# Kernel tuning notes

Measured on AMD Instinct MI355X. Metric: run time of the kernel, lower is better.

Reference implementation:

```python
import jax, jax.numpy as jnp
import numpy as np

TEMP = 0.05


def _l2norm(x, axis=-1, eps=1e-12):
    n = jnp.sqrt(jnp.sum(x * x, axis=axis, keepdims=True))
    return x / jnp.maximum(n, eps)


def setup_inputs() -> dict:
    key = jax.random.key(0)
    k1, k2, k3 = jax.random.split(key, 3)
    B, D, N = 1024, 2048, 16384
    inputs = jax.random.normal(k1, (B, D), dtype=jnp.float32)
    targets = jax.random.randint(k2, (B,), 0, N, dtype=jnp.int32).astype(jnp.int64)
    # cluster memory bank: initialized to unit-norm centroids (buffer is zeros in
    # torch but is always filled with normalized centroids before use)
    features = _l2norm(jax.random.normal(k3, (N, D), dtype=jnp.float32))
    return {"inputs": inputs, "targets": targets, "features": features}


def reference(inputs, targets, features):
    # ClusterMemory.forward: normalize -> cosine sim vs bank -> / temp
    xn = _l2norm(inputs, axis=1)            # [B, D]
    out = (xn @ features.T) / TEMP          # [B, N]
    return out
```

## Files before the change

### kernel.cpp

```cpp
#include <hip/hip_runtime.h>
#include <hip/hip_bf16.h>


typedef short bf16x8 __attribute__((ext_vector_type(8)));
typedef float f32x4  __attribute__((ext_vector_type(4)));

#define D_K   2048
#define N_N   16384
#define M_M   1024
#define TEMP_INV 20.0f

__device__ __forceinline__ unsigned short f2bf(float f) {
    unsigned u = __builtin_bit_cast(unsigned, f);
    u += 0x7FFFu + ((u >> 16) & 1u);
    return (unsigned short)(u >> 16);
}

#define GLOAD16(g, l) __builtin_amdgcn_global_load_lds(                        \
    (const __attribute__((address_space(1))) unsigned int*)(g),                \
    (__attribute__((address_space(3))) unsigned int*)(l), 16, 0, 0)

__global__ __launch_bounds__(256) void prep_kernel(const float* __restrict__ x,
                                                   const float* __restrict__ B,
                                                   unsigned short* __restrict__ abf,
                                                   unsigned short* __restrict__ bbf) {
    int t = threadIdx.x;
    if (blockIdx.x < M_M) {
        int row = blockIdx.x;
        const float4* xr = reinterpret_cast<const float4*>(x + (size_t)row * D_K);
        float4 a = xr[t * 2];
        float4 b = xr[t * 2 + 1];
        float s = a.x*a.x + a.y*a.y + a.z*a.z + a.w*a.w
                + b.x*b.x + b.y*b.y + b.z*b.z + b.w*b.w;
        #pragma unroll
        for (int off = 32; off > 0; off >>= 1) s += __shfl_down(s, off);
        __shared__ float ps[4];
        __shared__ float sbc;
        if ((t & 63) == 0) ps[t >> 6] = s;
        __syncthreads();
        if (t == 0) {
            float tot = ps[0] + ps[1] + ps[2] + ps[3];
            sbc = 1.0f / fmaxf(sqrtf(tot), 1e-12f);
        }
        __syncthreads();
        float rs = sbc;
        bf16x8 v;
        v[0] = (short)f2bf(a.x * rs); v[1] = (short)f2bf(a.y * rs);
        v[2] = (short)f2bf(a.z * rs); v[3] = (short)f2bf(a.w * rs);
        v[4] = (short)f2bf(b.x * rs); v[5] = (short)f2bf(b.y * rs);
        v[6] = (short)f2bf(b.z * rs); v[7] = (short)f2bf(b.w * rs);
        *reinterpret_cast<bf16x8*>(abf + (size_t)row * D_K + t * 8) = v;
    } else {
        const size_t nv = (size_t)N_N * D_K / 8;
        size_t stride = (size_t)(gridDim.x - M_M) * blockDim.x;
        for (size_t v = (size_t)(blockIdx.x - M_M) * blockDim.x + t; v < nv; v += stride) {
            const float4* p = reinterpret_cast<const float4*>(B) + v * 2;
            float4 a = p[0], b = p[1];
            bf16x8 o;
            o[0] = (short)f2bf(a.x); o[1] = (short)f2bf(a.y);
            o[2] = (short)f2bf(a.z); o[3] = (short)f2bf(a.w);
            o[4] = (short)f2bf(b.x); o[5] = (short)f2bf(b.y);
            o[6] = (short)f2bf(b.z); o[7] = (short)f2bf(b.w);
            reinterpret_cast<bf16x8*>(bbf)[v] = o;
        }
    }
}

__global__ __launch_bounds__(512, 2) void gemm8_kernel(const unsigned short* __restrict__ Abf,
                                                       const unsigned short* __restrict__ Bbf,
                                                       float* __restrict__ C) {
    __shared__ __align__(16) unsigned short lds[65536];

    int bid = blockIdx.x;
    int wg  = (bid & 7) * 32 + (bid >> 3);
    int tm  = wg & 3, tn = wg >> 2;
    int m_blk = tm * 256, n_blk = tn * 256;

    int t = threadIdx.x, lane = t & 63, w = t >> 6;
    int wm = w >> 2, wn = w & 3;

    int l15  = lane & 15;
    int slot = ((lane >> 4) ^ ((l15 >> 1) & 3)) * 16;
    int aoff = (wm * 128 + l15) * 64 + slot;
    int boff = (wn * 64  + l15) * 64 + slot;

    const unsigned short* gA[2];
    const unsigned short* gB[2];
    int sdst[2];
    #pragma unroll
    for (int pass = 0; pass < 2; ++pass) {
        int r = pass * 128 + (t >> 2);
        int csrc = (t & 3) ^ ((r >> 1) & 3);
        gA[pass] = Abf + (size_t)(m_blk + r) * D_K + csrc * 8;
        gB[pass] = Bbf + (size_t)(n_blk + r) * D_K + csrc * 8;
        sdst[pass] = pass * 8192 + w * 1024;
    }

    auto stage = [&](int mat, int s, int b, int ktile) {
        int kt = ktile < 32 ? ktile : 31;
        int koff = kt * 64 + s * 32;
        int ldsb = b * 65536 + mat * 32768 + s * 16384;
        GLOAD16((mat ? gB[0] : gA[0]) + koff, (char*)lds + ldsb + sdst[0]);
        GLOAD16((mat ? gB[1] : gA[1]) + koff, (char*)lds + ldsb + sdst[1]);
    };

    f32x4 acc[8][4] = {};
    bf16x8 bfr[4];

#define PHASE(b, mh, s, LOADB, stMat, stS, stB, stKt, VM)                      \
    {                                                                          \
        bf16x8 af[4];                                                          \
        _Pragma("unroll")                                                      \
        for (int f = 0; f < 4; ++f)                                            \
            af[f] = *reinterpret_cast<const bf16x8*>(                          \
                (char*)lds + (b) * 65536 + (s) * 16384 + aoff +                \
                ((mh) * 64 + f * 16) * 64);                                    \
        if (LOADB) {                                                           \
            _Pragma("unroll")                                                  \
            for (int n = 0; n < 4; ++n)                                        \
                bfr[n] = *reinterpret_cast<const bf16x8*>(                     \
                    (char*)lds + (b) * 65536 + 32768 + (s) * 16384 + boff +    \
                    n * 1024);                                                 \
        }                                                                      \
        stage(stMat, stS, stB, stKt);                                          \
        asm volatile("s_barrier" ::: "memory");                                \
        asm volatile("s_waitcnt lgkmcnt(0)" ::: "memory");                     \
        __builtin_amdgcn_sched_barrier(0);                                     \
        __builtin_amdgcn_s_setprio(1);                                         \
        _Pragma("unroll")                                                      \
        for (int f = 0; f < 4; ++f) {                                          \
            _Pragma("unroll")                                                  \
            for (int n = 0; n < 4; ++n)                                        \
                acc[(mh) * 4 + f][n] = __builtin_amdgcn_mfma_f32_16x16x32_bf16(\
                    af[f], bfr[n], acc[(mh) * 4 + f][n], 0, 0, 0);             \
        }                                                                      \
        __builtin_amdgcn_s_setprio(0);                                         \
        if (VM) asm volatile("s_waitcnt vmcnt(8)" ::: "memory");               \
        asm volatile("s_barrier" ::: "memory");                                \
    }

    stage(0, 0, 0, 0);
    stage(1, 0, 0, 0);
    stage(0, 1, 0, 0);
    stage(1, 1, 0, 0);
    stage(0, 0, 1, 1);
    stage(1, 0, 1, 1);
    asm volatile("s_waitcnt vmcnt(8)" ::: "memory");
    asm volatile("s_barrier" ::: "memory");

    for (int u = 0; u < 16; ++u) {
        int t1 = 2 * u + 1;
        PHASE(0, 0, 0, true,  0, 1, 1, t1,     false)
        PHASE(0, 1, 0, false, 1, 1, 1, t1,     true )
        PHASE(0, 0, 1, true,  0, 0, 0, t1 + 1, false)
        PHASE(0, 1, 1, false, 1, 0, 0, t1 + 1, true )
        PHASE(1, 0, 0, true,  0, 1, 0, t1 + 1, false)
        PHASE(1, 1, 0, false, 1, 1, 0, t1 + 1, true )
        PHASE(1, 0, 1, true,  0, 0, 1, t1 + 2, false)
        PHASE(1, 1, 1, false, 1, 0, 1, t1 + 2, true )
    }
#undef PHASE

    #pragma unroll
    for (int f = 0; f < 8; ++f) {
        int r = m_blk + wm * 128 + (f >> 2) * 64 + (f & 3) * 16 + (lane >> 4) * 4;
        #pragma unroll
        for (int j = 0; j < 4; ++j) {
            float* cp = C + (size_t)(r + j) * N_N + n_blk + wn * 64 + (lane & 15);
            #pragma unroll
            for (int n = 0; n < 4; ++n)
                cp[n * 16] = acc[f][n][j] * TEMP_INV;
        }
    }
}

__global__ __launch_bounds__(256) void rnorm_kernel(const float* __restrict__ x,
                                                    float* __restrict__ rn) {
    int row = blockIdx.x;
    const float4* xr = reinterpret_cast<const float4*>(x + (size_t)row * D_K);
    int t = threadIdx.x;
    float4 a = xr[t];
    float4 b = xr[t + 256];
    float s = a.x*a.x + a.y*a.y + a.z*a.z + a.w*a.w
            + b.x*b.x + b.y*b.y + b.z*b.z + b.w*b.w;
    #pragma unroll
    for (int off = 32; off > 0; off >>= 1) s += __shfl_down(s, off);
    __shared__ float ps[4];
    int wave = t >> 6, lane = t & 63;
    if (lane == 0) ps[wave] = s;
    __syncthreads();
    if (t == 0) {
        float tot = ps[0] + ps[1] + ps[2] + ps[3];
        rn[row] = 1.0f / fmaxf(sqrtf(tot), 1e-12f);
    }
}

__global__ __launch_bounds__(256, 2) void gemm_kernel(const float* __restrict__ A,
                                                      const float* __restrict__ Bm,
                                                      const float* __restrict__ rn,
                                                      float* __restrict__ C) {
    constexpr int BK = 64;
    __shared__ __align__(16) short lAs[128 * BK];
    __shared__ __align__(16) short lBs[128 * BK];
    int bid = blockIdx.x;
    int nb  = (bid & 7) * 128 + (bid >> 3);
    int tm  = nb & 7;
    int tn  = nb >> 3;
    int m0 = tm * 128, n0 = tn * 128;
    int t = threadIdx.x;
    int lane = t & 63, w = t >> 6;
    int wr = (w >> 1) * 64, wc = (w & 1) * 64;
    f32x4 acc[4][4] = {};
    float4 ra[4][2], rb[4][2];
    float  sc[4];
    int    srow[4], sgrp[4];
    #pragma unroll
    for (int i = 0; i < 4; ++i) {
        int li = t + i * 256;
        srow[i] = li >> 3;
        sgrp[i] = li & 7;
        sc[i]   = rn[m0 + srow[i]];
    }
    auto load_tiles = [&](int kt) {
        int k0 = kt * BK;
        #pragma unroll
        for (int i = 0; i < 4; ++i) {
            const float4* pa = reinterpret_cast<const float4*>(
                A + (size_t)(m0 + srow[i]) * D_K + k0 + sgrp[i] * 8);
            ra[i][0] = pa[0]; ra[i][1] = pa[1];
            const float4* pb = reinterpret_cast<const float4*>(
                Bm + (size_t)(n0 + srow[i]) * D_K + k0 + sgrp[i] * 8);
            rb[i][0] = pb[0]; rb[i][1] = pb[1];
        }
    };
    auto write_tiles = [&]() {
        #pragma unroll
        for (int i = 0; i < 4; ++i) {
            int row = srow[i];
            int slotw = sgrp[i] ^ (row & 7);
            float s = sc[i];
            bf16x8 va, vb;
            va[0] = (short)f2bf(ra[i][0].x * s); va[1] = (short)f2bf(ra[i][0].y * s);
            va[2] = (short)f2bf(ra[i][0].z * s); va[3] = (short)f2bf(ra[i][0].w * s);
            va[4] = (short)f2bf(ra[i][1].x * s); va[5] = (short)f2bf(ra[i][1].y * s);
            va[6] = (short)f2bf(ra[i][1].z * s); va[7] = (short)f2bf(ra[i][1].w * s);
        vb[0] = (short)f2bf(rb[i][0].x); vb[1] = (short)f2bf(rb[i][0].y);
        vb[2] = (short)f2bf(rb[i][0].z); vb[3] = (short)f2bf(rb[i][0].w);
        vb[4] = (short)f2bf(rb[i][1].x); vb[5] = (short)f2bf(rb[i][1].y);
        vb[6] = (short)f2bf(rb[i][1].z); vb[7] = (short)f2bf(rb[i][1].w);
            *reinterpret_cast<bf16x8*>(&lAs[row * BK + slotw * 8]) = va;
            *reinterpret_cast<bf16x8*>(&lBs[row * BK + slotw * 8]) = vb;
        }
    };
    auto compute = [&]() {
        #pragma unroll
        for (int ks = 0; ks < 2; ++ks) {
            bf16x8 af[4], bfr[4];
            #pragma unroll
            for (int f = 0; f < 4; ++f) {
                int arow = wr + f * 16 + (lane & 15);
                int aslot = (ks * 4 + (lane >> 4)) ^ (arow & 7);
                af[f] = *reinterpret_cast<const bf16x8*>(&lAs[arow * BK + aslot * 8]);
                int brow = wc + f * 16 + (lane & 15);
                int bslot = (ks * 4 + (lane >> 4)) ^ (brow & 7);
                bfr[f] = *reinterpret_cast<const bf16x8*>(&lBs[brow * BK + bslot * 8]);
            }
            #pragma unroll
            for (int m = 0; m < 4; ++m)
                #pragma unroll
                for (int n = 0; n < 4; ++n)
                    acc[m][n] = __builtin_amdgcn_mfma_f32_16x16x32_bf16(
                        af[m], bfr[n], acc[m][n], 0, 0, 0);
        }
    };
    load_tiles(0);
    write_tiles();
    for (int kt = 1; kt < D_K / BK; ++kt) {
        __syncthreads();
        load_tiles(kt);
        compute();
        __syncthreads();
        write_tiles();
    }
    __syncthreads();
    compute();
    #pragma unroll
    for (int m = 0; m < 4; ++m) {
        int r = m0 + wr + m * 16 + (lane >> 4) * 4;
        #pragma unroll
        for (int j = 0; j < 4; ++j) {
            float* cp = C + (size_t)(r + j) * N_N + n0 + wc + (lane & 15);
            #pragma unroll
            for (int n = 0; n < 4; ++n)
                cp[n * 16] = acc[m][n][j] * TEMP_INV;
        }
    }
}

extern "C" void kernel_launch(void* const* d_in, const int* in_sizes, int n_in,
                              void* d_out, int out_size, void* d_ws, size_t ws_size,
                              hipStream_t stream) {
    const float* inputs   = (const float*)d_in[0];
    const float* features = (const float*)d_in[2];
    float* out = (float*)d_out;

    const size_t needA = (size_t)M_M * D_K * 2;
    const size_t needB = (size_t)N_N * D_K * 2;
    if (ws_size >= needA + needB) {
        unsigned short* Abf = (unsigned short*)d_ws;
        unsigned short* Bbf = Abf + (size_t)M_M * D_K;
        prep_kernel<<<M_M + 2048, 256, 0, stream>>>(inputs, features, Abf, Bbf);
        gemm8_kernel<<<(M_M / 256) * (N_N / 256), 512, 0, stream>>>(Abf, Bbf, out);
    } else {
        float* rn = (float*)d_ws;
        rnorm_kernel<<<M_M, 256, 0, stream>>>(inputs, rn);
        gemm_kernel<<<(M_M / 128) * (N_N / 128), 256, 0, stream>>>(inputs, features, rn, out);
    }
}
```

Before: 103.8 us.

## Replace eight-phase interleaved GEMM pipeline with simple per-tile double-buffered loop

Replaces the fine-grained eight-phase schedule, which interleaved half-tile global-to-LDS loads with MFMA batches under setprio, with a simpler loop. Each iteration loads the full k-tile fragments from LDS, runs all 64 MFMAs, and then stages the next tile into the same buffer after a barrier. This cuts the barrier count and simplifies the schedule. In exchange it needs more registers for fragments and overlaps global loads with compute less finely, since loads are issued only after compute on that buffer finishes.

```diff
diff --git a/kernel.cpp b/kernel.cpp
--- a/kernel.cpp
+++ b/kernel.cpp
@@ -96,70 +96,67 @@
         sdst[pass] = pass * 8192 + w * 1024;
     }
 
-    auto stage = [&](int mat, int s, int b, int ktile) {
+    auto stageTile = [&](int b, int ktile) {
         int kt = ktile < 32 ? ktile : 31;
-        int koff = kt * 64 + s * 32;
-        int ldsb = b * 65536 + mat * 32768 + s * 16384;
-        GLOAD16((mat ? gB[0] : gA[0]) + koff, (char*)lds + ldsb + sdst[0]);
-        GLOAD16((mat ? gB[1] : gA[1]) + koff, (char*)lds + ldsb + sdst[1]);
+        #pragma unroll
+        for (int s = 0; s < 2; ++s) {
+            int koff = kt * 64 + s * 32;
+            GLOAD16(gA[0] + koff, (char*)lds + b * 65536 + s * 16384 + sdst[0]);
+            GLOAD16(gA[1] + koff, (char*)lds + b * 65536 + s * 16384 + sdst[1]);
+            GLOAD16(gB[0] + koff, (char*)lds + b * 65536 + 32768 + s * 16384 + sdst[0]);
+            GLOAD16(gB[1] + koff, (char*)lds + b * 65536 + 32768 + s * 16384 + sdst[1]);
+        }
     };
 
     f32x4 acc[8][4] = {};
-    bf16x8 bfr[4];
-
-#define PHASE(b, mh, s, LOADB, stMat, stS, stB, stKt, VM)                      \
-    {                                                                          \
-        bf16x8 af[4];                                                          \
-        _Pragma("unroll")                                                      \
-        for (int f = 0; f < 4; ++f)                                            \
-            af[f] = *reinterpret_cast<const bf16x8*>(                          \
-                (char*)lds + (b) * 65536 + (s) * 16384 + aoff +                \
-                ((mh) * 64 + f * 16) * 64);                                    \
-        if (LOADB) {                                                           \
-            _Pragma("unroll")                                                  \
-            for (int n = 0; n < 4; ++n)                                        \
-                bfr[n] = *reinterpret_cast<const bf16x8*>(                     \
-                    (char*)lds + (b) * 65536 + 32768 + (s) * 16384 + boff +    \
-                    n * 1024);                                                 \
-        }                                                                      \
-        stage(stMat, stS, stB, stKt);                                          \
-        asm volatile("s_barrier" ::: "memory");                                \
-        asm volatile("s_waitcnt lgkmcnt(0)" ::: "memory");                     \
-        __builtin_amdgcn_sched_barrier(0);                                     \
-        __builtin_amdgcn_s_setprio(1);                                         \
-        _Pragma("unroll")                                                      \
-        for (int f = 0; f < 4; ++f) {                                          \
-            _Pragma("unroll")                                                  \
-            for (int n = 0; n < 4; ++n)                                        \
-                acc[(mh) * 4 + f][n] = __builtin_amdgcn_mfma_f32_16x16x32_bf16(\
-                    af[f], bfr[n], acc[(mh) * 4 + f][n], 0, 0, 0);             \
-        }                                                                      \
-        __builtin_amdgcn_s_setprio(0);                                         \
-        if (VM) asm volatile("s_waitcnt vmcnt(8)" ::: "memory");               \
-        asm volatile("s_barrier" ::: "memory");                                \
-    }
-
-    stage(0, 0, 0, 0);
-    stage(1, 0, 0, 0);
-    stage(0, 1, 0, 0);
-    stage(1, 1, 0, 0);
-    stage(0, 0, 1, 1);
-    stage(1, 0, 1, 1);
+
+    stageTile(0, 0);
+    stageTile(1, 1);
     asm volatile("s_waitcnt vmcnt(8)" ::: "memory");
     asm volatile("s_barrier" ::: "memory");
 
-    for (int u = 0; u < 16; ++u) {
-        int t1 = 2 * u + 1;
-        PHASE(0, 0, 0, true,  0, 1, 1, t1,     false)
-        PHASE(0, 1, 0, false, 1, 1, 1, t1,     true )
-        PHASE(0, 0, 1, true,  0, 0, 0, t1 + 1, false)
-        PHASE(0, 1, 1, false, 1, 0, 0, t1 + 1, true )
-        PHASE(1, 0, 0, true,  0, 1, 0, t1 + 1, false)
-        PHASE(1, 1, 0, false, 1, 1, 0, t1 + 1, true )
-        PHASE(1, 0, 1, true,  0, 0, 1, t1 + 2, false)
-        PHASE(1, 1, 1, false, 1, 0, 1, t1 + 2, true )
-    }
-#undef PHASE
+    for (int T = 0; T < 32; ++T) {
+        int b = T & 1;
+        char* base = (char*)lds + b * 65536;
+
+        bf16x8 a0[8], b0[4], a1[8], b1[4];
+        #pragma unroll
+        for (int ff = 0; ff < 8; ++ff)
+            a0[ff] = *reinterpret_cast<const bf16x8*>(
+                base + aoff + (((ff >> 2) * 64 + (ff & 3) * 16) * 64));
+        #pragma unroll
+        for (int n = 0; n < 4; ++n)
+            b0[n] = *reinterpret_cast<const bf16x8*>(
+                base + 32768 + boff + n * 1024);
+        #pragma unroll
+        for (int ff = 0; ff < 8; ++ff)
+            a1[ff] = *reinterpret_cast<const bf16x8*>(
+                base + 16384 + aoff + (((ff >> 2) * 64 + (ff & 3) * 16) * 64));
+        #pragma unroll
+        for (int n = 0; n < 4; ++n)
+            b1[n] = *reinterpret_cast<const bf16x8*>(
+                base + 32768 + 16384 + boff + n * 1024);
+
+        #pragma unroll
+        for (int ff = 0; ff < 8; ++ff)
+            #pragma unroll
+            for (int n = 0; n < 4; ++n)
+                acc[ff][n] = __builtin_amdgcn_mfma_f32_16x16x32_bf16(
+                    a0[ff], b0[n], acc[ff][n], 0, 0, 0);
+        #pragma unroll
+        for (int ff = 0; ff < 8; ++ff)
+            #pragma unroll
+            for (int n = 0; n < 4; ++n)
+                acc[ff][n] = __builtin_amdgcn_mfma_f32_16x16x32_bf16(
+                    a1[ff], b1[n], acc[ff][n], 0, 0, 0);
+
+        asm volatile("s_waitcnt lgkmcnt(0)" ::: "memory");
+        __builtin_amdgcn_sched_barrier(0);
+        asm volatile("s_barrier" ::: "memory");
+        stageTile(b, T + 2);
+        asm volatile("s_waitcnt vmcnt(8)" ::: "memory");
+        asm volatile("s_barrier" ::: "memory");
+    }
 
     #pragma unroll
     for (int f = 0; f < 8; ++f) {
@@ -244,10 +241,10 @@
             va[2] = (short)f2bf(ra[i][0].z * s); va[3] = (short)f2bf(ra[i][0].w * s);
             va[4] = (short)f2bf(ra[i][1].x * s); va[5] = (short)f2bf(ra[i][1].y * s);
             va[6] = (short)f2bf(ra[i][1].z * s); va[7] = (short)f2bf(ra[i][1].w * s);
-        vb[0] = (short)f2bf(rb[i][0].x); vb[1] = (short)f2bf(rb[i][0].y);
-        vb[2] = (short)f2bf(rb[i][0].z); vb[3] = (short)f2bf(rb[i][0].w);
-        vb[4] = (short)f2bf(rb[i][1].x); vb[5] = (short)f2bf(rb[i][1].y);
-        vb[6] = (short)f2bf(rb[i][1].z); vb[7] = (short)f2bf(rb[i][1].w);
+            vb[0] = (short)f2bf(rb[i][0].x); vb[1] = (short)f2bf(rb[i][0].y);
+            vb[2] = (short)f2bf(rb[i][0].z); vb[3] = (short)f2bf(rb[i][0].w);
+            vb[4] = (short)f2bf(rb[i][1].x); vb[5] = (short)f2bf(rb[i][1].y);
+            vb[6] = (short)f2bf(rb[i][1].z); vb[7] = (short)f2bf(rb[i][1].w);
             *reinterpret_cast<bf16x8*>(&lAs[row * BK + slotw * 8]) = va;
             *reinterpret_cast<bf16x8*>(&lBs[row * BK + slotw * 8]) = vb;
         }
```

Result: slower. 116.4 us (+12.1%).

## Switch GEMM to 32x32x16 bf16 MFMA with fewer, coarser pipeline phases

Applied to the files above, without the earlier changes.

The main GEMM kernel now uses 32x32x16 bf16 MFMA instructions with 16-float accumulators in place of 16x16x32. Each wave covers its 128x64 tile with 4x2 blocks and reads operands for both k-halves per phase. The pipeline drops from eight phases per two k-tiles to two phases per k-tile, each issuing two stage loads and one barrier pair. This cuts LDS reads per MFMA and barrier count, at the cost of larger operand register use per phase and a less coalesced column-strided epilogue.

```diff
diff --git a/kernel.cpp b/kernel.cpp
--- a/kernel.cpp
+++ b/kernel.cpp
@@ -2,8 +2,9 @@
 #include <hip/hip_bf16.h>
 
 
-typedef short bf16x8 __attribute__((ext_vector_type(8)));
-typedef float f32x4  __attribute__((ext_vector_type(4)));
+typedef short  bf16x8 __attribute__((ext_vector_type(8)));
+typedef float  f32x4  __attribute__((ext_vector_type(4)));
+typedef float  f32x16 __attribute__((ext_vector_type(16)));
 
 #define D_K   2048
 #define N_N   16384
@@ -66,9 +67,9 @@
     }
 }
 
-__global__ __launch_bounds__(512, 2) void gemm8_kernel(const unsigned short* __restrict__ Abf,
-                                                       const unsigned short* __restrict__ Bbf,
-                                                       float* __restrict__ C) {
+__global__ __launch_bounds__(512, 2) void gemm32_kernel(const unsigned short* __restrict__ Abf,
+                                                        const unsigned short* __restrict__ Bbf,
+                                                        float* __restrict__ C) {
     __shared__ __align__(16) unsigned short lds[65536];
 
     int bid = blockIdx.x;
@@ -79,10 +80,15 @@
     int t = threadIdx.x, lane = t & 63, w = t >> 6;
     int wm = w >> 2, wn = w & 3;
 
-    int l15  = lane & 15;
-    int slot = ((lane >> 4) ^ ((l15 >> 1) & 3)) * 16;
-    int aoff = (wm * 128 + l15) * 64 + slot;
-    int boff = (wn * 64  + l15) * 64 + slot;
+    int row31 = lane & 31, khalf = lane >> 5;
+    int xorm  = (row31 >> 1) & 3;
+    int slotk[2], aao[4], bbo[2];
+    #pragma unroll
+    for (int kk = 0; kk < 2; ++kk) slotk[kk] = ((kk * 2 + khalf) ^ xorm) * 16;
+    #pragma unroll
+    for (int rb = 0; rb < 4; ++rb) aao[rb] = (wm * 128 + rb * 32 + row31) * 64;
+    #pragma unroll
+    for (int cb = 0; cb < 2; ++cb) bbo[cb] = (wn * 64 + cb * 32 + row31) * 64;
 
     const unsigned short* gA[2];
     const unsigned short* gB[2];
@@ -104,38 +110,41 @@
         GLOAD16((mat ? gB[1] : gA[1]) + koff, (char*)lds + ldsb + sdst[1]);
     };
 
-    f32x4 acc[8][4] = {};
-    bf16x8 bfr[4];
-
-#define PHASE(b, mh, s, LOADB, stMat, stS, stB, stKt, VM)                      \
+    f32x16 acc[4][2] = {};
+
+#define PHASE32(bb, ss, ST1, ST2)                                              \
     {                                                                          \
-        bf16x8 af[4];                                                          \
+        char* abase = (char*)lds + (bb) * 65536 + (ss) * 16384;                \
+        char* bbase = abase + 32768;                                           \
+        bf16x8 af[4][2], bv[2][2];                                             \
         _Pragma("unroll")                                                      \
-        for (int f = 0; f < 4; ++f)                                            \
-            af[f] = *reinterpret_cast<const bf16x8*>(                          \
-                (char*)lds + (b) * 65536 + (s) * 16384 + aoff +                \
-                ((mh) * 64 + f * 16) * 64);                                    \
-        if (LOADB) {                                                           \
+        for (int rb = 0; rb < 4; ++rb)                                         \
             _Pragma("unroll")                                                  \
-            for (int n = 0; n < 4; ++n)                                        \
-                bfr[n] = *reinterpret_cast<const bf16x8*>(                     \
-                    (char*)lds + (b) * 65536 + 32768 + (s) * 16384 + boff +    \
-                    n * 1024);                                                 \
-        }                                                                      \
-        stage(stMat, stS, stB, stKt);                                          \
+            for (int kk = 0; kk < 2; ++kk)                                     \
+                af[rb][kk] = *reinterpret_cast<const bf16x8*>(                 \
+                    abase + aao[rb] + slotk[kk]);                              \
+        _Pragma("unroll")                                                      \
+        for (int cb = 0; cb < 2; ++cb)                                         \
+            _Pragma("unroll")                                                  \
+            for (int kk = 0; kk < 2; ++kk)                                     \
+                bv[cb][kk] = *reinterpret_cast<const bf16x8*>(                 \
+                    bbase + bbo[cb] + slotk[kk]);                              \
+        ST1;                                                                   \
+        ST2;                                                                   \
         asm volatile("s_barrier" ::: "memory");                                \
         asm volatile("s_waitcnt lgkmcnt(0)" ::: "memory");                     \
         __builtin_amdgcn_sched_barrier(0);                                     \
         __builtin_amdgcn_s_setprio(1);                                         \
         _Pragma("unroll")                                                      \
-        for (int f = 0; f < 4; ++f) {                                          \
+        for (int kk = 0; kk < 2; ++kk)                                         \
             _Pragma("unroll")                                                  \
-            for (int n = 0; n < 4; ++n)                                        \
-                acc[(mh) * 4 + f][n] = __builtin_amdgcn_mfma_f32_16x16x32_bf16(\
-                    af[f], bfr[n], acc[(mh) * 4 + f][n], 0, 0, 0);             \
-        }                                                                      \
+            for (int rb = 0; rb < 4; ++rb)                                     \
+                _Pragma("unroll")                                              \
+                for (int cb = 0; cb < 2; ++cb)                                 \
+                    acc[rb][cb] = __builtin_amdgcn_mfma_f32_32x32x16_bf16(     \
+                        af[rb][kk], bv[cb][kk], acc[rb][cb], 0, 0, 0);         \
         __builtin_amdgcn_s_setprio(0);                                         \
-        if (VM) asm volatile("s_waitcnt vmcnt(8)" ::: "memory");               \
+        asm volatile("s_waitcnt vmcnt(8)" ::: "memory");                       \
         asm volatile("s_barrier" ::: "memory");                                \
     }
 
@@ -148,30 +157,25 @@
     asm volatile("s_waitcnt vmcnt(8)" ::: "memory");
     asm volatile("s_barrier" ::: "memory");
 
-    for (int u = 0; u < 16; ++u) {
-        int t1 = 2 * u + 1;
-        PHASE(0, 0, 0, true,  0, 1, 1, t1,     false)
-        PHASE(0, 1, 0, false, 1, 1, 1, t1,     true )
-        PHASE(0, 0, 1, true,  0, 0, 0, t1 + 1, false)
-        PHASE(0, 1, 1, false, 1, 0, 0, t1 + 1, true )
-        PHASE(1, 0, 0, true,  0, 1, 0, t1 + 1, false)
-        PHASE(1, 1, 0, false, 1, 1, 0, t1 + 1, true )
-        PHASE(1, 0, 1, true,  0, 0, 1, t1 + 2, false)
-        PHASE(1, 1, 1, false, 1, 0, 1, t1 + 2, true )
-    }
-#undef PHASE
-
-    #pragma unroll
-    for (int f = 0; f < 8; ++f) {
-        int r = m_blk + wm * 128 + (f >> 2) * 64 + (f & 3) * 16 + (lane >> 4) * 4;
-        #pragma unroll
-        for (int j = 0; j < 4; ++j) {
-            float* cp = C + (size_t)(r + j) * N_N + n_blk + wn * 64 + (lane & 15);
+    for (int T = 0; T < 32; ++T) {
+        int b = T & 1;
+        PHASE32(b, 0, stage(0, 1, b ^ 1, T + 1), stage(1, 1, b ^ 1, T + 1))
+        PHASE32(b, 1, stage(0, 0, b,     T + 2), stage(1, 0, b,     T + 2))
+    }
+#undef PHASE32
+
+    #pragma unroll
+    for (int rb = 0; rb < 4; ++rb)
+        #pragma unroll
+        for (int cb = 0; cb < 2; ++cb) {
+            int colg = n_blk + wn * 64 + cb * 32 + row31;
             #pragma unroll
-            for (int n = 0; n < 4; ++n)
-                cp[n * 16] = acc[f][n][j] * TEMP_INV;
-        }
-    }
+            for (int r = 0; r < 16; ++r) {
+                int rowg = m_blk + wm * 128 + rb * 32 +
+                           (r & 3) + 8 * (r >> 2) + 4 * khalf;
+                C[(size_t)rowg * N_N + colg] = acc[rb][cb][r] * TEMP_INV;
+            }
+        }
 }
 
 __global__ __launch_bounds__(256) void rnorm_kernel(const float* __restrict__ x,
@@ -244,10 +248,10 @@
             va[2] = (short)f2bf(ra[i][0].z * s); va[3] = (short)f2bf(ra[i][0].w * s);
             va[4] = (short)f2bf(ra[i][1].x * s); va[5] = (short)f2bf(ra[i][1].y * s);
             va[6] = (short)f2bf(ra[i][1].z * s); va[7] = (short)f2bf(ra[i][1].w * s);
-        vb[0] = (short)f2bf(rb[i][0].x); vb[1] = (short)f2bf(rb[i][0].y);
-        vb[2] = (short)f2bf(rb[i][0].z); vb[3] = (short)f2bf(rb[i][0].w);
-        vb[4] = (short)f2bf(rb[i][1].x); vb[5] = (short)f2bf(rb[i][1].y);
-        vb[6] = (short)f2bf(rb[i][1].z); vb[7] = (short)f2bf(rb[i][1].w);
+            vb[0] = (short)f2bf(rb[i][0].x); vb[1] = (short)f2bf(rb[i][0].y);
+            vb[2] = (short)f2bf(rb[i][0].z); vb[3] = (short)f2bf(rb[i][0].w);
+            vb[4] = (short)f2bf(rb[i][1].x); vb[5] = (short)f2bf(rb[i][1].y);
+            vb[6] = (short)f2bf(rb[i][1].z); vb[7] = (short)f2bf(rb[i][1].w);
             *reinterpret_cast<bf16x8*>(&lAs[row * BK + slotw * 8]) = va;
             *reinterpret_cast<bf16x8*>(&lBs[row * BK + slotw * 8]) = vb;
         }
@@ -310,7 +314,7 @@
         unsigned short* Abf = (unsigned short*)d_ws;
         unsigned short* Bbf = Abf + (size_t)M_M * D_K;
         prep_kernel<<<M_M + 2048, 256, 0, stream>>>(inputs, features, Abf, Bbf);
-        gemm8_kernel<<<(M_M / 256) * (N_N / 256), 512, 0, stream>>>(Abf, Bbf, out);
+        gemm32_kernel<<<(M_M / 256) * (N_N / 256), 512, 0, stream>>>(Abf, Bbf, out);
     } else {
         float* rn = (float*)d_ws;
         rnorm_kernel<<<M_M, 256, 0, stream>>>(inputs, rn);
```

Result: slower. 113.2 us (+9.0%).

## Restructure GEMM main loop into four coarser phases per K-tile pair

Applied to the files above, without the earlier changes.

Replaces the eight-phase ping-pong schedule, which split each k-substep into two M halves, with four phases. Each phase loads all eight A fragments and four B fragments, issues both A and B stage loads, and runs 32 MFMAs. This halves the number of barriers and waitcnt points per K tile, reducing sync overhead. In exchange it holds more fragment registers live, which may pressure occupancy at 2 waves/SIMD, and gives coarser overlap between loads and MFMAs.

```diff
diff --git a/kernel.cpp b/kernel.cpp
--- a/kernel.cpp
+++ b/kernel.cpp
@@ -66,7 +66,7 @@
     }
 }
 
-__global__ __launch_bounds__(512, 2) void gemm8_kernel(const unsigned short* __restrict__ Abf,
+__global__ __launch_bounds__(512, 2) void gemm4_kernel(const unsigned short* __restrict__ Abf,
                                                        const unsigned short* __restrict__ Bbf,
                                                        float* __restrict__ C) {
     __shared__ __align__(16) unsigned short lds[65536];
@@ -81,8 +81,11 @@
 
     int l15  = lane & 15;
     int slot = ((lane >> 4) ^ ((l15 >> 1) & 3)) * 16;
-    int aoff = (wm * 128 + l15) * 64 + slot;
-    int boff = (wn * 64  + l15) * 64 + slot;
+    int aoff[8], boff;
+    #pragma unroll
+    for (int f = 0; f < 8; ++f)
+        aoff[f] = (wm * 128 + f * 16 + l15) * 64 + slot;
+    boff = (wn * 64 + l15) * 64 + slot;
 
     const unsigned short* gA[2];
     const unsigned short* gB[2];
@@ -105,37 +108,34 @@
     };
 
     f32x4 acc[8][4] = {};
-    bf16x8 bfr[4];
-
-#define PHASE(b, mh, s, LOADB, stMat, stS, stB, stKt, VM)                      \
+
+#define PHASE4(b, s, stS, stB, stKt)                                           \
     {                                                                          \
-        bf16x8 af[4];                                                          \
+        bf16x8 af[8], bfr[4];                                                  \
         _Pragma("unroll")                                                      \
-        for (int f = 0; f < 4; ++f)                                            \
+        for (int f = 0; f < 8; ++f)                                            \
             af[f] = *reinterpret_cast<const bf16x8*>(                          \
-                (char*)lds + (b) * 65536 + (s) * 16384 + aoff +                \
-                ((mh) * 64 + f * 16) * 64);                                    \
-        if (LOADB) {                                                           \
-            _Pragma("unroll")                                                  \
-            for (int n = 0; n < 4; ++n)                                        \
-                bfr[n] = *reinterpret_cast<const bf16x8*>(                     \
-                    (char*)lds + (b) * 65536 + 32768 + (s) * 16384 + boff +    \
-                    n * 1024);                                                 \
-        }                                                                      \
-        stage(stMat, stS, stB, stKt);                                          \
+                (char*)lds + (b) * 65536 + (s) * 16384 + aoff[f]);             \
+        _Pragma("unroll")                                                      \
+        for (int n = 0; n < 4; ++n)                                            \
+            bfr[n] = *reinterpret_cast<const bf16x8*>(                         \
+                (char*)lds + (b) * 65536 + 32768 + (s) * 16384 + boff +        \
+                n * 1024);                                                     \
+        stage(0, stS, stB, stKt);                                              \
+        stage(1, stS, stB, stKt);                                              \
         asm volatile("s_barrier" ::: "memory");                                \
         asm volatile("s_waitcnt lgkmcnt(0)" ::: "memory");                     \
         __builtin_amdgcn_sched_barrier(0);                                     \
         __builtin_amdgcn_s_setprio(1);                                         \
         _Pragma("unroll")                                                      \
-        for (int f = 0; f < 4; ++f) {                                          \
+        for (int f = 0; f < 8; ++f) {                                          \
             _Pragma("unroll")                                                  \
             for (int n = 0; n < 4; ++n)                                        \
-                acc[(mh) * 4 + f][n] = __builtin_amdgcn_mfma_f32_16x16x32_bf16(\
-                    af[f], bfr[n], acc[(mh) * 4 + f][n], 0, 0, 0);             \
+                acc[f][n] = __builtin_amdgcn_mfma_f32_16x16x32_bf16(           \
+                    af[f], bfr[n], acc[f][n], 0, 0, 0);                        \
         }                                                                      \
         __builtin_amdgcn_s_setprio(0);                                         \
-        if (VM) asm volatile("s_waitcnt vmcnt(8)" ::: "memory");               \
+        asm volatile("s_waitcnt vmcnt(8)" ::: "memory");                       \
         asm volatile("s_barrier" ::: "memory");                                \
     }
 
@@ -148,25 +148,19 @@
     asm volatile("s_waitcnt vmcnt(8)" ::: "memory");
     asm volatile("s_barrier" ::: "memory");
 
-    for (int u = 0; u < 16; ++u) {
-        int t1 = 2 * u + 1;
-        PHASE(0, 0, 0, true,  0, 1, 1, t1,     false)
-        PHASE(0, 1, 0, false, 1, 1, 1, t1,     true )
-        PHASE(0, 0, 1, true,  0, 0, 0, t1 + 1, false)
-        PHASE(0, 1, 1, false, 1, 0, 0, t1 + 1, true )
-        PHASE(1, 0, 0, true,  0, 1, 0, t1 + 1, false)
-        PHASE(1, 1, 0, false, 1, 1, 0, t1 + 1, true )
-        PHASE(1, 0, 1, true,  0, 0, 1, t1 + 2, false)
-        PHASE(1, 1, 1, false, 1, 0, 1, t1 + 2, true )
-    }
-#undef PHASE
+    for (int T = 0; T < 32; ++T) {
+        int b = T & 1;
+        PHASE4(b, 0, 1, b ^ 1, T + 1)
+        PHASE4(b, 1, 0, b,     T + 2)
+    }
+#undef PHASE4
 
     #pragma unroll
     for (int f = 0; f < 8; ++f) {
-        int r = m_blk + wm * 128 + (f >> 2) * 64 + (f & 3) * 16 + (lane >> 4) * 4;
+        int r = m_blk + wm * 128 + f * 16 + (lane >> 4) * 4;
         #pragma unroll
         for (int j = 0; j < 4; ++j) {
-            float* cp = C + (size_t)(r + j) * N_N + n_blk + wn * 64 + (lane & 15);
+            float* cp = C + (size_t)(r + j) * N_N + n_blk + wn * 64 + l15;
             #pragma unroll
             for (int n = 0; n < 4; ++n)
                 cp[n * 16] = acc[f][n][j] * TEMP_INV;
@@ -244,10 +238,10 @@
             va[2] = (short)f2bf(ra[i][0].z * s); va[3] = (short)f2bf(ra[i][0].w * s);
             va[4] = (short)f2bf(ra[i][1].x * s); va[5] = (short)f2bf(ra[i][1].y * s);
             va[6] = (short)f2bf(ra[i][1].z * s); va[7] = (short)f2bf(ra[i][1].w * s);
-        vb[0] = (short)f2bf(rb[i][0].x); vb[1] = (short)f2bf(rb[i][0].y);
-        vb[2] = (short)f2bf(rb[i][0].z); vb[3] = (short)f2bf(rb[i][0].w);
-        vb[4] = (short)f2bf(rb[i][1].x); vb[5] = (short)f2bf(rb[i][1].y);
-        vb[6] = (short)f2bf(rb[i][1].z); vb[7] = (short)f2bf(rb[i][1].w);
+            vb[0] = (short)f2bf(rb[i][0].x); vb[1] = (short)f2bf(rb[i][0].y);
+            vb[2] = (short)f2bf(rb[i][0].z); vb[3] = (short)f2bf(rb[i][0].w);
+            vb[4] = (short)f2bf(rb[i][1].x); vb[5] = (short)f2bf(rb[i][1].y);
+            vb[6] = (short)f2bf(rb[i][1].z); vb[7] = (short)f2bf(rb[i][1].w);
             *reinterpret_cast<bf16x8*>(&lAs[row * BK + slotw * 8]) = va;
             *reinterpret_cast<bf16x8*>(&lBs[row * BK + slotw * 8]) = vb;
         }
@@ -310,7 +304,7 @@
         unsigned short* Abf = (unsigned short*)d_ws;
         unsigned short* Bbf = Abf + (size_t)M_M * D_K;
         prep_kernel<<<M_M + 2048, 256, 0, stream>>>(inputs, features, Abf, Bbf);
-        gemm8_kernel<<<(M_M / 256) * (N_N / 256), 512, 0, stream>>>(Abf, Bbf, out);
+        gemm4_kernel<<<(M_M / 256) * (N_N / 256), 512, 0, stream>>>(Abf, Bbf, out);
     } else {
         float* rn = (float*)d_ws;
         rnorm_kernel<<<M_M, 256, 0, stream>>>(inputs, rn);
```

Result: slower. 106.5 us (+2.7%).
